# Kernel tuning notes

Measured on AMD Instinct MI355X. Metric: run time of the kernel, lower is better.

The kernel has to match this reference:

```python
import jax, jax.numpy as jnp
import numpy as np

N, F, V, E = 16384, 39, 100000, 16
H1, H2 = 400, 400
EPS = 1e-5

def setup_inputs() -> dict:
    key = jax.random.key(0)
    ks = jax.random.split(key, 12)
    xi = jax.random.randint(ks[0], (N, F, 1), 0, V)  # indices per field
    xv = jax.random.uniform(ks[1], (N, F), dtype=jnp.float32)
    # stacked per-field embedding tables (each table has V+1 rows)
    emb1 = jax.random.normal(ks[2], (F, V + 1), dtype=jnp.float32)          # 1st-order
    emb2 = jax.random.normal(ks[3], (F, V + 1, E), dtype=jnp.float32)       # 2nd-order
    D = F * E
    W1 = jax.random.normal(ks[4], (D, H1), dtype=jnp.float32) / np.sqrt(D)
    b1 = jnp.zeros((H1,), jnp.float32)
    g1 = jnp.ones((H1,), jnp.float32)
    be1 = jnp.zeros((H1,), jnp.float32)
    W2 = jax.random.normal(ks[5], (H1, H2), dtype=jnp.float32) / np.sqrt(H1)
    b2 = jnp.zeros((H2,), jnp.float32)
    g2 = jnp.ones((H2,), jnp.float32)
    be2 = jnp.zeros((H2,), jnp.float32)
    bias = jax.random.normal(ks[6], (1,), dtype=jnp.float32)
    return dict(xi=xi, xv=xv, emb1=emb1, emb2=emb2, W1=W1, b1=b1, g1=g1, be1=be1,
                W2=W2, b2=b2, g2=g2, be2=be2, bias=bias)

def _batchnorm(x, g, b):
    # BatchNorm1d in training mode: batch mean/var (biased)
    mu = x.mean(0)
    var = x.var(0)
    return g * (x - mu) * jax.lax.rsqrt(var + EPS) + b

def reference(xi, xv, emb1, emb2, W1, b1, g1, be1, W2, b2, g2, be2, bias):
    idx = xi[:, :, 0]                     # (N, F)
    f_ids = jnp.arange(F)[None, :]        # (1, F)
    e1 = emb1[f_ids, idx] * xv            # (N, F): per-field 1st-order term
    e2 = emb2[f_ids, idx] * xv[:, :, None]  # (N, F, E)
    s = e2.sum(axis=1)                    # (N, E) sum of embeddings
    fm2 = 0.5 * (s * s - (e2 * e2).sum(axis=1))  # (N, E) FM 2nd-order
    deep = e2.reshape(e2.shape[0], F * E)
    h = _batchnorm(deep @ W1 + b1, g1, be1)       # dropout = identity (eval)
    h = _batchnorm(h @ W2 + b2, g2, be2)
    return e1.sum(axis=1) + fm2.sum(axis=1) + h.sum(axis=1) + bias[0]
```

## Files before the change

### kernel.cpp

```cpp
#include <hip/hip_runtime.h>
#include <hip/hip_bf16.h>

#define Nn 16384
#define Ff 39
#define Vv 100000
#define Ee 16
#define Dd 624
#define KP1 640
#define KP2 448
#define Hh 400
#define EPSf 1e-5f

typedef short short8 __attribute__((ext_vector_type(8)));
typedef float floatx4 __attribute__((ext_vector_type(4)));

__device__ __forceinline__ unsigned short f2bu(float x) {
  __hip_bfloat16 h = __float2bfloat16(x);
  return *reinterpret_cast<unsigned short*>(&h);
}
__device__ __forceinline__ float bf2f(unsigned short v) {
  union { unsigned int u; float f; } x; x.u = ((unsigned int)v) << 16; return x.f;
}

__device__ __forceinline__ void gload16(void* lds, const void* g) {
  __builtin_amdgcn_global_load_lds(
      (const __attribute__((address_space(1))) unsigned int*)g,
      (__attribute__((address_space(3))) unsigned int*)lds, 16, 0, 0);
}

__global__ __launch_bounds__(256) void embed_kernel(
    const int* __restrict__ xi, const float* __restrict__ xv,
    const float* __restrict__ emb1, const float* __restrict__ emb2,
    const float* __restrict__ bias, const float* __restrict__ W1,
    __hip_bfloat16* __restrict__ deep, float* __restrict__ p,
    __hip_bfloat16* __restrict__ W1t, float* __restrict__ stats,
    __hip_bfloat16* __restrict__ x1b) {
  const int b = blockIdx.x;
  __shared__ float Tt[64][65];
  __shared__ int   sidx[4][40];
  __shared__ float sxv[4][40];
  if (b < 70) {
    const int tk = b / 7, tn = b % 7;
    const int k0 = tk * 64, n0 = tn * 64;
    const int c = threadIdx.x & 63, r0 = (threadIdx.x >> 6) * 16;
    const int n = n0 + c;
    #pragma unroll
    for (int r = r0; r < r0 + 16; ++r) {
      const int k = k0 + r;
      Tt[c][r] = (k < Dd && n < Hh) ? W1[(size_t)k * Hh + n] : 0.f;
    }
    __syncthreads();
    const int nl = threadIdx.x >> 2, kq = (threadIdx.x & 3) * 16;
    const int nw = n0 + nl;
    if (nw < Hh) {
      #pragma unroll
      for (int q = 0; q < 4; ++q) {
        const int kk = kq + q * 4;
        *(ushort4*)&W1t[(size_t)nw * KP1 + k0 + kk] = make_ushort4(
            f2bu(Tt[nl][kk]), f2bu(Tt[nl][kk + 1]),
            f2bu(Tt[nl][kk + 2]), f2bu(Tt[nl][kk + 3]));
      }
    }
    return;
  }
  if (b == 70) {
    for (int i = threadIdx.x; i < 2000; i += 256) stats[i] = 0.f;
    return;
  }
  const int w = threadIdx.x >> 6;
  const int lane = threadIdx.x & 63;
  const int n = (b - 71) * 4 + w;
  if (lane < Ff) {
    sidx[w][lane] = xi[n * Ff + lane];
    sxv[w][lane]  = xv[n * Ff + lane];
  }
  __syncthreads();

  float e1v = 0.f;
  if (lane < Ff)
    e1v = emb1[(long)lane * (Vv + 1) + sidx[w][lane]] * sxv[w][lane];

  const float4* e2v = (const float4*)emb2;
  float se0 = 0.f, se1 = 0.f, se2 = 0.f, se3 = 0.f;
  float qe0 = 0.f, qe1 = 0.f, qe2 = 0.f, qe3 = 0.f;
  #pragma unroll
  for (int t = 0; t < 3; ++t) {
    const int j4 = lane + t * 64;
    if (j4 < 156) {
      const int f = j4 >> 2;
      float4 v = e2v[((long)f * (Vv + 1) + sidx[w][f]) * 4 + (j4 & 3)];
      const float xf = sxv[w][f];
      v.x *= xf; v.y *= xf; v.z *= xf; v.w *= xf;
      *(ushort4*)&deep[(size_t)n * KP1 + j4 * 4] =
          make_ushort4(f2bu(v.x), f2bu(v.y), f2bu(v.z), f2bu(v.w));
      se0 += v.x; qe0 += v.x * v.x;
      se1 += v.y; qe1 += v.y * v.y;
      se2 += v.z; qe2 += v.z * v.z;
      se3 += v.w; qe3 += v.w * v.w;
    }
  }
  if (lane < 4)  *(ushort4*)&deep[(size_t)n * KP1 + Dd + lane * 4] = make_ushort4(0, 0, 0, 0);
  if (lane < 12) *(ushort4*)&x1b [(size_t)n * KP2 + Hh + lane * 4] = make_ushort4(0, 0, 0, 0);

  #pragma unroll
  for (int d = 4; d < 64; d <<= 1) {
    se0 += __shfl_xor(se0, d); qe0 += __shfl_xor(qe0, d);
    se1 += __shfl_xor(se1, d); qe1 += __shfl_xor(qe1, d);
    se2 += __shfl_xor(se2, d); qe2 += __shfl_xor(qe2, d);
    se3 += __shfl_xor(se3, d); qe3 += __shfl_xor(qe3, d);
  }
  float val = 0.f;
  if (lane < 4)
    val = 0.5f * ((se0 * se0 - qe0) + (se1 * se1 - qe1) +
                  (se2 * se2 - qe2) + (se3 * se3 - qe3));
  val += e1v;
  #pragma unroll
  for (int d = 1; d < 64; d <<= 1) val += __shfl_xor(val, d);
  if (lane == 0) p[n] = val + bias[0];
}

__global__ __launch_bounds__(256) void gemm_bf16(
    const __hip_bfloat16* __restrict__ A, const __hip_bfloat16* __restrict__ Wt,
    const float* __restrict__ bias, __hip_bfloat16* __restrict__ C,
    float* __restrict__ s, float* __restrict__ ss, const int K, const int ldc) {
  __shared__ __align__(16) short As_s[128 * 64];
  __shared__ __align__(16) short Bs_s[80 * 64];
  __shared__ float redS[4][5][16], redQ[4][5][16];
  const int tid = threadIdx.x;
  const int lin = blockIdx.x + blockIdx.y * 5;
  const int v   = (lin & 7) * 80 + (lin >> 3);
  const int n0  = (v % 5) * 80;
  const int m0  = (v / 5) * 128;
  const int w = tid >> 6, lane = tid & 63;
  const int lm = lane & 15, qd = lane >> 4;

  floatx4 acc[2][5];
  #pragma unroll
  for (int i = 0; i < 2; ++i)
    #pragma unroll
    for (int j = 0; j < 5; ++j)
      acc[i][j] = (floatx4){0.f, 0.f, 0.f, 0.f};

  const int nk = K >> 6;
  for (int ks = 0; ks < nk; ++ks) {
    const int k0 = ks << 6;
    #pragma unroll
    for (int j = 0; j < 4; ++j) {
      const int c = tid + j * 256;
      const int m = c >> 3, kc = c & 7;
      gload16(&As_s[c * 8], &A[(size_t)(m0 + m) * K + k0 + ((kc ^ (m & 7)) << 3)]);
    }
    #pragma unroll
    for (int j = 0; j < 3; ++j) {
      const int c = tid + j * 256;
      if (c < 640) {
        const int nn = c >> 3, kc = c & 7;
        gload16(&Bs_s[c * 8], &Wt[(size_t)(n0 + nn) * K + k0 + ((kc ^ (nn & 7)) << 3)]);
      }
    }
    __syncthreads();
    #pragma unroll
    for (int h = 0; h < 2; ++h) {
      const int sl = (h * 32 + qd * 8) >> 3;
      const int r0 = w * 32 + lm, r1 = r0 + 16;
      const short8 a0 = *(const short8*)&As_s[r0 * 64 + ((sl ^ (r0 & 7)) << 3)];
      const short8 a1 = *(const short8*)&As_s[r1 * 64 + ((sl ^ (r1 & 7)) << 3)];
      #pragma unroll
      for (int nt = 0; nt < 5; ++nt) {
        const int rn = nt * 16 + lm;
        const short8 bfr = *(const short8*)&Bs_s[rn * 64 + ((sl ^ (rn & 7)) << 3)];
        acc[0][nt] = __builtin_amdgcn_mfma_f32_16x16x32_bf16(a0, bfr, acc[0][nt], 0, 0, 0);
        acc[1][nt] = __builtin_amdgcn_mfma_f32_16x16x32_bf16(a1, bfr, acc[1][nt], 0, 0, 0);
      }
    }
    __syncthreads();
  }

  const int rb = m0 + w * 32 + qd * 4;
  #pragma unroll
  for (int nt = 0; nt < 5; ++nt) {
    const int col = n0 + nt * 16 + lm;
    const float bc = bias[col];
    float cs = 0.f, cq = 0.f;
    #pragma unroll
    for (int mt = 0; mt < 2; ++mt) {
      #pragma unroll
      for (int r = 0; r < 4; ++r) {
        const float vv = acc[mt][nt][r] + bc;
        float vf = vv;
        if (C) {
          const __hip_bfloat16 hv = __float2bfloat16(vv);
          C[(size_t)(rb + mt * 16 + r) * ldc + col] = hv;
          vf = __bfloat162float(hv);
        }
        cs += vf; cq += vf * vf;
      }
    }
    cs += __shfl_xor(cs, 16); cq += __shfl_xor(cq, 16);
    cs += __shfl_xor(cs, 32); cq += __shfl_xor(cq, 32);
    if (lane < 16) { redS[w][nt][lm] = cs; redQ[w][nt][lm] = cq; }
  }
  __syncthreads();
  if (tid < 80) {
    const int nt = tid >> 4, l = tid & 15;
    const int col = n0 + nt * 16 + l;
    atomicAdd(&s[col],  redS[0][nt][l] + redS[1][nt][l] + redS[2][nt][l] + redS[3][nt][l]);
    atomicAdd(&ss[col], redQ[0][nt][l] + redQ[1][nt][l] + redQ[2][nt][l] + redQ[3][nt][l]);
  }
}

__global__ __launch_bounds__(256) void prep2_kernel(
    const float* __restrict__ W2,
    const float* __restrict__ s1, const float* __restrict__ ss1,
    const float* __restrict__ g1, const float* __restrict__ be1,
    const float* __restrict__ b2, __hip_bfloat16* __restrict__ W2t, float* __restrict__ b2p) {
  __shared__ float sa[64], sc[64];
  __shared__ float Tt[64][65];
  __shared__ float pcs[256];
  const int tb = blockIdx.x;
  const int tk = tb / 7, tn = tb % 7;
  const int k0 = tk * 64, n0 = tn * 64;
  const int t = threadIdx.x;
  if (t < 64) {
    const int k = k0 + t;
    float a = 0.f, cv = 0.f;
    if (k < Hh) {
      const float mu = s1[k] * (1.f / Nn);
      const float var = ss1[k] * (1.f / Nn) - mu * mu;
      a = g1[k] * rsqrtf(var + EPSf);
      cv = be1[k] - a * mu;
    }
    sa[t] = a; sc[t] = cv;
  }
  __syncthreads();
  const int c = t & 63, r0 = (t >> 6) * 16;
  const int n = n0 + c;
  float pc = 0.f;
  #pragma unroll
  for (int r = r0; r < r0 + 16; ++r) {
    const int k = k0 + r;
    const float wv = (k < Hh && n < Hh) ? W2[(size_t)k * Hh + n] : 0.f;
    Tt[c][r] = sa[r] * wv;
    pc += sc[r] * wv;
  }
  pcs[t] = pc;
  __syncthreads();
  if (t < 64 && n0 + t < Hh) {
    float tot = pcs[t] + pcs[t + 64] + pcs[t + 128] + pcs[t + 192];
    if (k0 == 0) tot += b2[n0 + t];
    atomicAdd(&b2p[n0 + t], tot);
  }
  const int nl = t >> 2, kq = (t & 3) * 16;
  const int nw = n0 + nl;
  if (nw < Hh) {
    #pragma unroll
    for (int q = 0; q < 4; ++q) {
      const int kk = kq + q * 4;
      *(ushort4*)&W2t[(size_t)nw * KP2 + k0 + kk] = make_ushort4(
          f2bu(Tt[nl][kk]), f2bu(Tt[nl][kk + 1]),
          f2bu(Tt[nl][kk + 2]), f2bu(Tt[nl][kk + 3]));
    }
  }
}

__global__ __launch_bounds__(256) void prep3_kernel(
    const __hip_bfloat16* __restrict__ W2t,
    const float* __restrict__ s2, const float* __restrict__ ss2,
    const float* __restrict__ g2, const float* __restrict__ be2,
    const float* __restrict__ b2p, float* __restrict__ u) {
  __shared__ float sal[Hh];
  __shared__ float part[4][64];
  __shared__ float red[256];
  const int t = threadIdx.x;
  float cpart = 0.f;
  for (int h = t; h < Hh; h += 256) {
    const float mu = s2[h] * (1.f / Nn);
    const float var = ss2[h] * (1.f / Nn) - mu * mu;
    const float al = g2[h] * rsqrtf(var + EPSf);
    sal[h] = al;
    cpart += be2[h] - al * mu + al * b2p[h];
  }
  __syncthreads();
  const int k = blockIdx.x * 64 + (t & 63);
  const int hs = t >> 6;
  float acc = 0.f;
  for (int h = hs * 100; h < hs * 100 + 100; ++h)
    acc += sal[h] * bf2f(*(const unsigned short*)&W2t[(size_t)h * KP2 + k]);
  part[hs][t & 63] = acc;
  __syncthreads();
  if (t < 64) u[blockIdx.x * 64 + t] = part[0][t] + part[1][t] + part[2][t] + part[3][t];
  if (blockIdx.x == 0) {
    red[t] = cpart;
    __syncthreads();
    for (int d = 128; d > 0; d >>= 1) { if (t < d) red[t] += red[t + d]; __syncthreads(); }
    if (t == 0) u[KP2] = red[0];
  }
}

__global__ __launch_bounds__(256) void final_kernel(
    const __hip_bfloat16* __restrict__ x1, const float* __restrict__ u,
    const float* __restrict__ p, float* __restrict__ out) {
  __shared__ float su[KP2];
  __shared__ float scc;
  const int t = threadIdx.x;
  for (int i = t; i < KP2; i += 256) su[i] = u[i];
  if (t == 0) scc = u[KP2];
  __syncthreads();
  const int w = t >> 6, lane = t & 63;
  const int n = blockIdx.x * 4 + w;
  const unsigned short* row = (const unsigned short*)(x1 + (size_t)n * KP2);
  float acc = 0.f;
  #pragma unroll
  for (int h0 = lane * 4; h0 < KP2; h0 += 256) {
    const ushort4 uv = *(const ushort4*)&row[h0];
    acc += bf2f(uv.x) * su[h0]     + bf2f(uv.y) * su[h0 + 1]
         + bf2f(uv.z) * su[h0 + 2] + bf2f(uv.w) * su[h0 + 3];
  }
  #pragma unroll
  for (int d = 1; d < 64; d <<= 1) acc += __shfl_xor(acc, d);
  if (lane == 0) out[n] = p[n] + acc + scc;
}

extern "C" void kernel_launch(void* const* d_in, const int* in_sizes, int n_in,
                              void* d_out, int out_size, void* d_ws, size_t ws_size,
                              hipStream_t stream) {
  const int*   xi   = (const int*)d_in[0];
  const float* xv   = (const float*)d_in[1];
  const float* emb1 = (const float*)d_in[2];
  const float* emb2 = (const float*)d_in[3];
  const float* W1   = (const float*)d_in[4];
  const float* b1   = (const float*)d_in[5];
  const float* g1   = (const float*)d_in[6];
  const float* be1  = (const float*)d_in[7];
  const float* W2   = (const float*)d_in[8];
  const float* b2   = (const float*)d_in[9];
  const float* g2   = (const float*)d_in[10];
  const float* be2  = (const float*)d_in[11];
  const float* bias = (const float*)d_in[12];
  float* out = (float*)d_out;

  char* ws = (char*)d_ws;
  __hip_bfloat16* deep = (__hip_bfloat16*)ws;  ws += (size_t)Nn * KP1 * 2;
  __hip_bfloat16* x1b  = (__hip_bfloat16*)ws;  ws += (size_t)Nn * KP2 * 2;
  __hip_bfloat16* W1t  = (__hip_bfloat16*)ws;  ws += (size_t)Hh * KP1 * 2;
  __hip_bfloat16* W2t  = (__hip_bfloat16*)ws;  ws += (size_t)Hh * KP2 * 2;
  float* p    = (float*)ws;  ws += (size_t)Nn * 4;
  float* s1   = (float*)ws;  ws += Hh * 4;
  float* ss1  = (float*)ws;  ws += Hh * 4;
  float* s2   = (float*)ws;  ws += Hh * 4;
  float* ss2  = (float*)ws;  ws += Hh * 4;
  float* b2p  = (float*)ws;  ws += Hh * 4;
  float* u    = (float*)ws;  ws += (KP2 + 1) * 4;

  embed_kernel<<<4167, 256, 0, stream>>>(xi, xv, emb1, emb2, bias, W1, deep, p, W1t, s1, x1b);
  gemm_bf16<<<dim3(5, Nn / 128), 256, 0, stream>>>(deep, W1t, b1, x1b, s1, ss1, KP1, KP2);
  prep2_kernel<<<49, 256, 0, stream>>>(W2, s1, ss1, g1, be1, b2, W2t, b2p);
  gemm_bf16<<<dim3(5, Nn / 128), 256, 0, stream>>>(x1b, W2t, b2p, nullptr, s2, ss2, KP2, 0);
  prep3_kernel<<<7, 256, 0, stream>>>(W2t, s2, ss2, g2, be2, b2p, u);
  final_kernel<<<Nn / 4, 256, 0, stream>>>(x1b, u, p, out);
}
```

Before: 387.7 us.

## Fuse all stages into one persistent kernel with software grid barriers

Replaces the six separate kernel launches with a single persistent kernel of 512 blocks. Atomic-counter grid barriers separate the embedding, first GEMM, BN prep, second GEMM, second prep and final reduction phases. Stats and barrier counters are zeroed with a memset before the launch. The aim is to remove launch gaps and tail effects between stages. In exchange, each phase gets a fixed grid (640 GEMM tiles over 512 blocks leaves an uneven second wave), and the spin barriers need all blocks to be co-resident.

```diff
diff --git a/kernel.cpp b/kernel.cpp
--- a/kernel.cpp
+++ b/kernel.cpp
@@ -10,6 +10,7 @@
 #define KP2 448
 #define Hh 400
 #define EPSf 1e-5f
+#define GRIDB 512
 
 typedef short short8 __attribute__((ext_vector_type(8)));
 typedef float floatx4 __attribute__((ext_vector_type(4)));
@@ -21,116 +22,39 @@
 __device__ __forceinline__ float bf2f(unsigned short v) {
   union { unsigned int u; float f; } x; x.u = ((unsigned int)v) << 16; return x.f;
 }
-
 __device__ __forceinline__ void gload16(void* lds, const void* g) {
   __builtin_amdgcn_global_load_lds(
       (const __attribute__((address_space(1))) unsigned int*)g,
       (__attribute__((address_space(3))) unsigned int*)lds, 16, 0, 0);
 }
 
-__global__ __launch_bounds__(256) void embed_kernel(
-    const int* __restrict__ xi, const float* __restrict__ xv,
-    const float* __restrict__ emb1, const float* __restrict__ emb2,
-    const float* __restrict__ bias, const float* __restrict__ W1,
-    __hip_bfloat16* __restrict__ deep, float* __restrict__ p,
-    __hip_bfloat16* __restrict__ W1t, float* __restrict__ stats,
-    __hip_bfloat16* __restrict__ x1b) {
-  const int b = blockIdx.x;
-  __shared__ float Tt[64][65];
-  __shared__ int   sidx[4][40];
-  __shared__ float sxv[4][40];
-  if (b < 70) {
-    const int tk = b / 7, tn = b % 7;
-    const int k0 = tk * 64, n0 = tn * 64;
-    const int c = threadIdx.x & 63, r0 = (threadIdx.x >> 6) * 16;
-    const int n = n0 + c;
-    #pragma unroll
-    for (int r = r0; r < r0 + 16; ++r) {
-      const int k = k0 + r;
-      Tt[c][r] = (k < Dd && n < Hh) ? W1[(size_t)k * Hh + n] : 0.f;
-    }
-    __syncthreads();
-    const int nl = threadIdx.x >> 2, kq = (threadIdx.x & 3) * 16;
-    const int nw = n0 + nl;
-    if (nw < Hh) {
-      #pragma unroll
-      for (int q = 0; q < 4; ++q) {
-        const int kk = kq + q * 4;
-        *(ushort4*)&W1t[(size_t)nw * KP1 + k0 + kk] = make_ushort4(
-            f2bu(Tt[nl][kk]), f2bu(Tt[nl][kk + 1]),
-            f2bu(Tt[nl][kk + 2]), f2bu(Tt[nl][kk + 3]));
-      }
-    }
-    return;
-  }
-  if (b == 70) {
-    for (int i = threadIdx.x; i < 2000; i += 256) stats[i] = 0.f;
-    return;
-  }
-  const int w = threadIdx.x >> 6;
-  const int lane = threadIdx.x & 63;
-  const int n = (b - 71) * 4 + w;
-  if (lane < Ff) {
-    sidx[w][lane] = xi[n * Ff + lane];
-    sxv[w][lane]  = xv[n * Ff + lane];
-  }
-  __syncthreads();
-
-  float e1v = 0.f;
-  if (lane < Ff)
-    e1v = emb1[(long)lane * (Vv + 1) + sidx[w][lane]] * sxv[w][lane];
-
-  const float4* e2v = (const float4*)emb2;
-  float se0 = 0.f, se1 = 0.f, se2 = 0.f, se3 = 0.f;
-  float qe0 = 0.f, qe1 = 0.f, qe2 = 0.f, qe3 = 0.f;
-  #pragma unroll
-  for (int t = 0; t < 3; ++t) {
-    const int j4 = lane + t * 64;
-    if (j4 < 156) {
-      const int f = j4 >> 2;
-      float4 v = e2v[((long)f * (Vv + 1) + sidx[w][f]) * 4 + (j4 & 3)];
-      const float xf = sxv[w][f];
-      v.x *= xf; v.y *= xf; v.z *= xf; v.w *= xf;
-      *(ushort4*)&deep[(size_t)n * KP1 + j4 * 4] =
-          make_ushort4(f2bu(v.x), f2bu(v.y), f2bu(v.z), f2bu(v.w));
-      se0 += v.x; qe0 += v.x * v.x;
-      se1 += v.y; qe1 += v.y * v.y;
-      se2 += v.z; qe2 += v.z * v.z;
-      se3 += v.w; qe3 += v.w * v.w;
-    }
-  }
-  if (lane < 4)  *(ushort4*)&deep[(size_t)n * KP1 + Dd + lane * 4] = make_ushort4(0, 0, 0, 0);
-  if (lane < 12) *(ushort4*)&x1b [(size_t)n * KP2 + Hh + lane * 4] = make_ushort4(0, 0, 0, 0);
-
-  #pragma unroll
-  for (int d = 4; d < 64; d <<= 1) {
-    se0 += __shfl_xor(se0, d); qe0 += __shfl_xor(qe0, d);
-    se1 += __shfl_xor(se1, d); qe1 += __shfl_xor(qe1, d);
-    se2 += __shfl_xor(se2, d); qe2 += __shfl_xor(qe2, d);
-    se3 += __shfl_xor(se3, d); qe3 += __shfl_xor(qe3, d);
-  }
-  float val = 0.f;
-  if (lane < 4)
-    val = 0.5f * ((se0 * se0 - qe0) + (se1 * se1 - qe1) +
-                  (se2 * se2 - qe2) + (se3 * se3 - qe3));
-  val += e1v;
-  #pragma unroll
-  for (int d = 1; d < 64; d <<= 1) val += __shfl_xor(val, d);
-  if (lane == 0) p[n] = val + bias[0];
-}
-
-__global__ __launch_bounds__(256) void gemm_bf16(
+__device__ __forceinline__ void gridbar(unsigned* bar, int id) {
+  __syncthreads();
+  if (threadIdx.x == 0) {
+    __threadfence();
+    unsigned prev = atomicAdd(&bar[id], 1u);
+    if (prev + 1u < (unsigned)GRIDB) {
+      while (atomicAdd(&bar[id], 0u) < (unsigned)GRIDB)
+        __builtin_amdgcn_s_sleep(2);
+    }
+    __threadfence();
+  }
+  __syncthreads();
+}
+
+__device__ __forceinline__ void gemm_body(
     const __hip_bfloat16* __restrict__ A, const __hip_bfloat16* __restrict__ Wt,
     const float* __restrict__ bias, __hip_bfloat16* __restrict__ C,
-    float* __restrict__ s, float* __restrict__ ss, const int K, const int ldc) {
-  __shared__ __align__(16) short As_s[128 * 64];
-  __shared__ __align__(16) short Bs_s[80 * 64];
-  __shared__ float redS[4][5][16], redQ[4][5][16];
+    float* __restrict__ s, float* __restrict__ ss, const int K, const int ldc,
+    char* smem, const int tile) {
+  short* As_s = (short*)smem;
+  short* Bs_s = (short*)(smem + 16384);
+  float* redS = (float*)(smem + 16384 + 10240);
+  float* redQ = redS + 320;
   const int tid = threadIdx.x;
-  const int lin = blockIdx.x + blockIdx.y * 5;
-  const int v   = (lin & 7) * 80 + (lin >> 3);
-  const int n0  = (v % 5) * 80;
-  const int m0  = (v / 5) * 128;
+  const int v  = (tile & 7) * 80 + (tile >> 3);
+  const int n0 = (v % 5) * 80;
+  const int m0 = (v / 5) * 128;
   const int w = tid >> 6, lane = tid & 63;
   const int lm = lane & 15, qd = lane >> 4;
 
@@ -161,7 +85,7 @@
     __syncthreads();
     #pragma unroll
     for (int h = 0; h < 2; ++h) {
-      const int sl = (h * 32 + qd * 8) >> 3;
+      const int sl = h * 4 + qd;
       const int r0 = w * 32 + lm, r1 = r0 + 16;
       const short8 a0 = *(const short8*)&As_s[r0 * 64 + ((sl ^ (r0 & 7)) << 3)];
       const short8 a1 = *(const short8*)&As_s[r1 * 64 + ((sl ^ (r1 & 7)) << 3)];
@@ -198,26 +122,26 @@
     }
     cs += __shfl_xor(cs, 16); cq += __shfl_xor(cq, 16);
     cs += __shfl_xor(cs, 32); cq += __shfl_xor(cq, 32);
-    if (lane < 16) { redS[w][nt][lm] = cs; redQ[w][nt][lm] = cq; }
+    if (lane < 16) { redS[w * 80 + nt * 16 + lm] = cs; redQ[w * 80 + nt * 16 + lm] = cq; }
   }
   __syncthreads();
   if (tid < 80) {
     const int nt = tid >> 4, l = tid & 15;
     const int col = n0 + nt * 16 + l;
-    atomicAdd(&s[col],  redS[0][nt][l] + redS[1][nt][l] + redS[2][nt][l] + redS[3][nt][l]);
-    atomicAdd(&ss[col], redQ[0][nt][l] + redQ[1][nt][l] + redQ[2][nt][l] + redQ[3][nt][l]);
-  }
-}
-
-__global__ __launch_bounds__(256) void prep2_kernel(
-    const float* __restrict__ W2,
-    const float* __restrict__ s1, const float* __restrict__ ss1,
-    const float* __restrict__ g1, const float* __restrict__ be1,
-    const float* __restrict__ b2, __hip_bfloat16* __restrict__ W2t, float* __restrict__ b2p) {
-  __shared__ float sa[64], sc[64];
-  __shared__ float Tt[64][65];
-  __shared__ float pcs[256];
-  const int tb = blockIdx.x;
+    const int o = nt * 16 + l;
+    atomicAdd(&s[col],  redS[o] + redS[80 + o] + redS[160 + o] + redS[240 + o]);
+    atomicAdd(&ss[col], redQ[o] + redQ[80 + o] + redQ[160 + o] + redQ[240 + o]);
+  }
+}
+
+__device__ __forceinline__ void prep2_body(
+    const float* __restrict__ W2, const float* __restrict__ s1, const float* __restrict__ ss1,
+    const float* __restrict__ g1, const float* __restrict__ be1, const float* __restrict__ b2,
+    __hip_bfloat16* __restrict__ W2t, float* __restrict__ b2p, char* smem, const int tb) {
+  float* sa = (float*)smem;
+  float* sc = sa + 64;
+  float (*Tt)[65] = (float(*)[65])(smem + 512);
+  float* pcs = (float*)(smem + 512 + 16640);
   const int tk = tb / 7, tn = tb % 7;
   const int k0 = tk * 64, n0 = tn * 64;
   const int t = threadIdx.x;
@@ -263,14 +187,14 @@
   }
 }
 
-__global__ __launch_bounds__(256) void prep3_kernel(
-    const __hip_bfloat16* __restrict__ W2t,
-    const float* __restrict__ s2, const float* __restrict__ ss2,
-    const float* __restrict__ g2, const float* __restrict__ be2,
-    const float* __restrict__ b2p, float* __restrict__ u) {
-  __shared__ float sal[Hh];
-  __shared__ float part[4][64];
-  __shared__ float red[256];
+__device__ __forceinline__ void prep3_body(
+    const __hip_bfloat16* __restrict__ W2t, const float* __restrict__ s2,
+    const float* __restrict__ ss2, const float* __restrict__ g2,
+    const float* __restrict__ be2, const float* __restrict__ b2p,
+    float* __restrict__ u, char* smem, const int blk) {
+  float* sal  = (float*)smem;
+  float* part = sal + Hh;
+  float* red  = part + 256;
   const int t = threadIdx.x;
   float cpart = 0.f;
   for (int h = t; h < Hh; h += 256) {
@@ -281,15 +205,15 @@
     cpart += be2[h] - al * mu + al * b2p[h];
   }
   __syncthreads();
-  const int k = blockIdx.x * 64 + (t & 63);
+  const int k = blk * 64 + (t & 63);
   const int hs = t >> 6;
   float acc = 0.f;
   for (int h = hs * 100; h < hs * 100 + 100; ++h)
     acc += sal[h] * bf2f(*(const unsigned short*)&W2t[(size_t)h * KP2 + k]);
-  part[hs][t & 63] = acc;
-  __syncthreads();
-  if (t < 64) u[blockIdx.x * 64 + t] = part[0][t] + part[1][t] + part[2][t] + part[3][t];
-  if (blockIdx.x == 0) {
+  part[hs * 64 + (t & 63)] = acc;
+  __syncthreads();
+  if (t < 64) u[blk * 64 + t] = part[t] + part[64 + t] + part[128 + t] + part[192 + t];
+  if (blk == 0) {
     red[t] = cpart;
     __syncthreads();
     for (int d = 128; d > 0; d >>= 1) { if (t < d) red[t] += red[t + d]; __syncthreads(); }
@@ -297,28 +221,143 @@
   }
 }
 
-__global__ __launch_bounds__(256) void final_kernel(
-    const __hip_bfloat16* __restrict__ x1, const float* __restrict__ u,
-    const float* __restrict__ p, float* __restrict__ out) {
-  __shared__ float su[KP2];
-  __shared__ float scc;
-  const int t = threadIdx.x;
-  for (int i = t; i < KP2; i += 256) su[i] = u[i];
-  if (t == 0) scc = u[KP2];
-  __syncthreads();
-  const int w = t >> 6, lane = t & 63;
-  const int n = blockIdx.x * 4 + w;
-  const unsigned short* row = (const unsigned short*)(x1 + (size_t)n * KP2);
-  float acc = 0.f;
-  #pragma unroll
-  for (int h0 = lane * 4; h0 < KP2; h0 += 256) {
-    const ushort4 uv = *(const ushort4*)&row[h0];
-    acc += bf2f(uv.x) * su[h0]     + bf2f(uv.y) * su[h0 + 1]
-         + bf2f(uv.z) * su[h0 + 2] + bf2f(uv.w) * su[h0 + 3];
-  }
-  #pragma unroll
-  for (int d = 1; d < 64; d <<= 1) acc += __shfl_xor(acc, d);
-  if (lane == 0) out[n] = p[n] + acc + scc;
+__global__ __launch_bounds__(256, 2) void fused(
+    const int* __restrict__ xi, const float* __restrict__ xv,
+    const float* __restrict__ emb1, const float* __restrict__ emb2,
+    const float* __restrict__ W1, const float* __restrict__ b1,
+    const float* __restrict__ g1, const float* __restrict__ be1,
+    const float* __restrict__ W2, const float* __restrict__ b2,
+    const float* __restrict__ g2, const float* __restrict__ be2,
+    const float* __restrict__ bias, float* __restrict__ out,
+    __hip_bfloat16* __restrict__ deep, __hip_bfloat16* __restrict__ x1b,
+    __hip_bfloat16* __restrict__ W1t, __hip_bfloat16* __restrict__ W2t,
+    float* __restrict__ p, float* __restrict__ stats, float* __restrict__ u,
+    unsigned* __restrict__ bar) {
+  __shared__ __align__(16) char smem[29184];
+  const int blk = blockIdx.x, tid = threadIdx.x;
+  const int w = tid >> 6, lane = tid & 63;
+  float* s1  = stats;
+  float* ss1 = stats + 400;
+  float* s2  = stats + 800;
+  float* ss2 = stats + 1200;
+  float* b2p = stats + 1600;
+
+  if (blk < 70) {
+    float (*Tt)[65] = (float(*)[65])smem;
+    const int tk = blk / 7, tn = blk % 7;
+    const int k0 = tk * 64, n0 = tn * 64;
+    const int c = tid & 63, r0 = (tid >> 6) * 16;
+    const int n = n0 + c;
+    #pragma unroll
+    for (int r = r0; r < r0 + 16; ++r) {
+      const int k = k0 + r;
+      Tt[c][r] = (k < Dd && n < Hh) ? W1[(size_t)k * Hh + n] : 0.f;
+    }
+    __syncthreads();
+    const int nl = tid >> 2, kq = (tid & 3) * 16;
+    const int nw = n0 + nl;
+    if (nw < Hh) {
+      #pragma unroll
+      for (int q = 0; q < 4; ++q) {
+        const int kk = kq + q * 4;
+        *(ushort4*)&W1t[(size_t)nw * KP1 + k0 + kk] = make_ushort4(
+            f2bu(Tt[nl][kk]), f2bu(Tt[nl][kk + 1]),
+            f2bu(Tt[nl][kk + 2]), f2bu(Tt[nl][kk + 3]));
+      }
+    }
+  }
+  {
+    int*   sidx = (int*)smem;
+    float* sxv  = (float*)(smem + 640);
+    const float4* e2v = (const float4*)emb2;
+    const float bias0 = bias[0];
+    for (int g = blk; g < 4096; g += GRIDB) {
+      __syncthreads();
+      const int n = g * 4 + w;
+      if (lane < Ff) {
+        sidx[w * 40 + lane] = xi[n * Ff + lane];
+        sxv [w * 40 + lane] = xv[n * Ff + lane];
+      }
+      __syncthreads();
+      float e1v = 0.f;
+      if (lane < Ff)
+        e1v = emb1[(long)lane * (Vv + 1) + sidx[w * 40 + lane]] * sxv[w * 40 + lane];
+
+      float se0 = 0.f, se1 = 0.f, se2 = 0.f, se3 = 0.f;
+      float qe0 = 0.f, qe1 = 0.f, qe2 = 0.f, qe3 = 0.f;
+      #pragma unroll
+      for (int t = 0; t < 3; ++t) {
+        const int j4 = lane + t * 64;
+        if (j4 < 156) {
+          const int f = j4 >> 2;
+          float4 v = e2v[((long)f * (Vv + 1) + sidx[w * 40 + f]) * 4 + (j4 & 3)];
+          const float xf = sxv[w * 40 + f];
+          v.x *= xf; v.y *= xf; v.z *= xf; v.w *= xf;
+          *(ushort4*)&deep[(size_t)n * KP1 + j4 * 4] =
+              make_ushort4(f2bu(v.x), f2bu(v.y), f2bu(v.z), f2bu(v.w));
+          se0 += v.x; qe0 += v.x * v.x;
+          se1 += v.y; qe1 += v.y * v.y;
+          se2 += v.z; qe2 += v.z * v.z;
+          se3 += v.w; qe3 += v.w * v.w;
+        }
+      }
+      if (lane < 4)  *(ushort4*)&deep[(size_t)n * KP1 + Dd + lane * 4] = make_ushort4(0, 0, 0, 0);
+      if (lane < 12) *(ushort4*)&x1b [(size_t)n * KP2 + Hh + lane * 4] = make_ushort4(0, 0, 0, 0);
+
+      #pragma unroll
+      for (int d = 4; d < 64; d <<= 1) {
+        se0 += __shfl_xor(se0, d); qe0 += __shfl_xor(qe0, d);
+        se1 += __shfl_xor(se1, d); qe1 += __shfl_xor(qe1, d);
+        se2 += __shfl_xor(se2, d); qe2 += __shfl_xor(qe2, d);
+        se3 += __shfl_xor(se3, d); qe3 += __shfl_xor(qe3, d);
+      }
+      float val = 0.f;
+      if (lane < 4)
+        val = 0.5f * ((se0 * se0 - qe0) + (se1 * se1 - qe1) +
+                      (se2 * se2 - qe2) + (se3 * se3 - qe3));
+      val += e1v;
+      #pragma unroll
+      for (int d = 1; d < 64; d <<= 1) val += __shfl_xor(val, d);
+      if (lane == 0) p[n] = val + bias0;
+    }
+  }
+  gridbar(bar, 0);
+
+  for (int t = blk; t < 640; t += GRIDB)
+    gemm_body(deep, W1t, b1, x1b, s1, ss1, KP1, KP2, smem, t);
+  gridbar(bar, 1);
+
+  if (blk < 49) prep2_body(W2, s1, ss1, g1, be1, b2, W2t, b2p, smem, blk);
+  gridbar(bar, 2);
+
+  for (int t = blk; t < 640; t += GRIDB)
+    gemm_body(x1b, W2t, b2p, nullptr, s2, ss2, KP2, 0, smem, t);
+  gridbar(bar, 3);
+
+  if (blk < 7) prep3_body(W2t, s2, ss2, g2, be2, b2p, u, smem, blk);
+  gridbar(bar, 4);
+
+  {
+    float* su = (float*)smem;
+    __syncthreads();
+    for (int i = tid; i < KP2 + 1; i += 256) su[i] = u[i];
+    __syncthreads();
+    const float cc = su[KP2];
+    for (int g = blk; g < 4096; g += GRIDB) {
+      const int n = g * 4 + w;
+      const unsigned short* row = (const unsigned short*)(x1b + (size_t)n * KP2);
+      float acc = 0.f;
+      #pragma unroll
+      for (int h0 = lane * 4; h0 < KP2; h0 += 256) {
+        const ushort4 uv = *(const ushort4*)&row[h0];
+        acc += bf2f(uv.x) * su[h0]     + bf2f(uv.y) * su[h0 + 1]
+             + bf2f(uv.z) * su[h0 + 2] + bf2f(uv.w) * su[h0 + 3];
+      }
+      #pragma unroll
+      for (int d = 1; d < 64; d <<= 1) acc += __shfl_xor(acc, d);
+      if (lane == 0) out[n] = p[n] + acc + cc;
+    }
+  }
 }
 
 extern "C" void kernel_launch(void* const* d_in, const int* in_sizes, int n_in,
@@ -344,18 +383,13 @@
   __hip_bfloat16* x1b  = (__hip_bfloat16*)ws;  ws += (size_t)Nn * KP2 * 2;
   __hip_bfloat16* W1t  = (__hip_bfloat16*)ws;  ws += (size_t)Hh * KP1 * 2;
   __hip_bfloat16* W2t  = (__hip_bfloat16*)ws;  ws += (size_t)Hh * KP2 * 2;
-  float* p    = (float*)ws;  ws += (size_t)Nn * 4;
-  float* s1   = (float*)ws;  ws += Hh * 4;
-  float* ss1  = (float*)ws;  ws += Hh * 4;
-  float* s2   = (float*)ws;  ws += Hh * 4;
-  float* ss2  = (float*)ws;  ws += Hh * 4;
-  float* b2p  = (float*)ws;  ws += Hh * 4;
-  float* u    = (float*)ws;  ws += (KP2 + 1) * 4;
-
-  embed_kernel<<<4167, 256, 0, stream>>>(xi, xv, emb1, emb2, bias, W1, deep, p, W1t, s1, x1b);
-  gemm_bf16<<<dim3(5, Nn / 128), 256, 0, stream>>>(deep, W1t, b1, x1b, s1, ss1, KP1, KP2);
-  prep2_kernel<<<49, 256, 0, stream>>>(W2, s1, ss1, g1, be1, b2, W2t, b2p);
-  gemm_bf16<<<dim3(5, Nn / 128), 256, 0, stream>>>(x1b, W2t, b2p, nullptr, s2, ss2, KP2, 0);
-  prep3_kernel<<<7, 256, 0, stream>>>(W2t, s2, ss2, g2, be2, b2p, u);
-  final_kernel<<<Nn / 4, 256, 0, stream>>>(x1b, u, p, out);
-}
+  float* p     = (float*)ws;  ws += (size_t)Nn * 4;
+  float* stats = (float*)ws;  ws += 2000 * 4;
+  float* u     = (float*)ws;  ws += 449 * 4;
+  unsigned* bar = (unsigned*)ws; ws += 8 * 4;
+
+  hipMemsetAsync(stats, 0, (2000 + 449 + 8) * 4, stream);
+  fused<<<GRIDB, 256, 0, stream>>>(xi, xv, emb1, emb2, W1, b1, g1, be1,
+                                   W2, b2, g2, be2, bias, out,
+                                   deep, x1b, W1t, W2t, p, stats, u, bar);
+}
```

Result: slower. 587.4 us (+51.5%).

## Fold BN-prep kernels into GEMM launches as tail blocks gated by completion counter

Applied to the files above, without the earlier changes.

Removes the separate prep2 and prep3 launches by appending extra blocks to each GEMM grid. Those blocks spin on an atomic done counter until all 640 tile blocks have published their column statistics, then run the prep work. The goal is to save two kernel launches and their inter-kernel gaps. The risk is spin-waiting blocks occupying CUs, and deadlock if the tail blocks were ever scheduled before the work blocks. Shared memory is unified into one char buffer and the stats layout is contiguous so a single zeroing pass also clears the counters.

```diff
diff --git a/kernel.cpp b/kernel.cpp
--- a/kernel.cpp
+++ b/kernel.cpp
@@ -10,6 +10,7 @@
 #define KP2 448
 #define Hh 400
 #define EPSf 1e-5f
+#define NWORK 640
 
 typedef short short8 __attribute__((ext_vector_type(8)));
 typedef float floatx4 __attribute__((ext_vector_type(4)));
@@ -21,7 +22,6 @@
 __device__ __forceinline__ float bf2f(unsigned short v) {
   union { unsigned int u; float f; } x; x.u = ((unsigned int)v) << 16; return x.f;
 }
-
 __device__ __forceinline__ void gload16(void* lds, const void* g) {
   __builtin_amdgcn_global_load_lds(
       (const __attribute__((address_space(1))) unsigned int*)g,
@@ -64,7 +64,7 @@
     return;
   }
   if (b == 70) {
-    for (int i = threadIdx.x; i < 2000; i += 256) stats[i] = 0.f;
+    for (int i = threadIdx.x; i < 2008; i += 256) stats[i] = 0.f;
     return;
   }
   const int w = threadIdx.x >> 6;
@@ -119,15 +119,124 @@
   if (lane == 0) p[n] = val + bias[0];
 }
 
+__device__ __forceinline__ void prep2_body(
+    const float* __restrict__ W2, const float* __restrict__ s1, const float* __restrict__ ss1,
+    const float* __restrict__ g1, const float* __restrict__ be1, const float* __restrict__ b2,
+    __hip_bfloat16* __restrict__ W2t, float* __restrict__ b2p, char* smem, const int tb) {
+  float* sa = (float*)smem;
+  float* sc = sa + 64;
+  float (*Tt)[65] = (float(*)[65])(smem + 512);
+  float* pcs = (float*)(smem + 512 + 16640);
+  const int tk = tb / 7, tn = tb % 7;
+  const int k0 = tk * 64, n0 = tn * 64;
+  const int t = threadIdx.x;
+  if (t < 64) {
+    const int k = k0 + t;
+    float a = 0.f, cv = 0.f;
+    if (k < Hh) {
+      const float mu = s1[k] * (1.f / Nn);
+      const float var = ss1[k] * (1.f / Nn) - mu * mu;
+      a = g1[k] * rsqrtf(var + EPSf);
+      cv = be1[k] - a * mu;
+    }
+    sa[t] = a; sc[t] = cv;
+  }
+  __syncthreads();
+  const int c = t & 63, r0 = (t >> 6) * 16;
+  const int n = n0 + c;
+  float pc = 0.f;
+  #pragma unroll
+  for (int r = r0; r < r0 + 16; ++r) {
+    const int k = k0 + r;
+    const float wv = (k < Hh && n < Hh) ? W2[(size_t)k * Hh + n] : 0.f;
+    Tt[c][r] = sa[r] * wv;
+    pc += sc[r] * wv;
+  }
+  pcs[t] = pc;
+  __syncthreads();
+  if (t < 64 && n0 + t < Hh) {
+    float tot = pcs[t] + pcs[t + 64] + pcs[t + 128] + pcs[t + 192];
+    if (k0 == 0) tot += b2[n0 + t];
+    atomicAdd(&b2p[n0 + t], tot);
+  }
+  const int nl = t >> 2, kq = (t & 3) * 16;
+  const int nw = n0 + nl;
+  if (nw < Hh) {
+    #pragma unroll
+    for (int q = 0; q < 4; ++q) {
+      const int kk = kq + q * 4;
+      *(ushort4*)&W2t[(size_t)nw * KP2 + k0 + kk] = make_ushort4(
+          f2bu(Tt[nl][kk]), f2bu(Tt[nl][kk + 1]),
+          f2bu(Tt[nl][kk + 2]), f2bu(Tt[nl][kk + 3]));
+    }
+  }
+}
+
+__device__ __forceinline__ void prep3_body(
+    const __hip_bfloat16* __restrict__ W2t, const float* __restrict__ s2,
+    const float* __restrict__ ss2, const float* __restrict__ g2,
+    const float* __restrict__ be2, const float* __restrict__ b2p,
+    float* __restrict__ u, char* smem, const int blk) {
+  float* sal  = (float*)smem;
+  float* part = sal + Hh;
+  float* red  = part + 256;
+  const int t = threadIdx.x;
+  float cpart = 0.f;
+  for (int h = t; h < Hh; h += 256) {
+    const float mu = s2[h] * (1.f / Nn);
+    const float var = ss2[h] * (1.f / Nn) - mu * mu;
+    const float al = g2[h] * rsqrtf(var + EPSf);
+    sal[h] = al;
+    cpart += be2[h] - al * mu + al * b2p[h];
+  }
+  __syncthreads();
+  const int k = blk * 64 + (t & 63);
+  const int hs = t >> 6;
+  float acc = 0.f;
+  for (int h = hs * 100; h < hs * 100 + 100; ++h)
+    acc += sal[h] * bf2f(*(const unsigned short*)&W2t[(size_t)h * KP2 + k]);
+  part[hs * 64 + (t & 63)] = acc;
+  __syncthreads();
+  if (t < 64) u[blk * 64 + t] = part[t] + part[64 + t] + part[128 + t] + part[192 + t];
+  if (blk == 0) {
+    red[t] = cpart;
+    __syncthreads();
+    for (int d = 128; d > 0; d >>= 1) { if (t < d) red[t] += red[t + d]; __syncthreads(); }
+    if (t == 0) u[KP2] = red[0];
+  }
+}
+
 __global__ __launch_bounds__(256) void gemm_bf16(
     const __hip_bfloat16* __restrict__ A, const __hip_bfloat16* __restrict__ Wt,
     const float* __restrict__ bias, __hip_bfloat16* __restrict__ C,
-    float* __restrict__ s, float* __restrict__ ss, const int K, const int ldc) {
-  __shared__ __align__(16) short As_s[128 * 64];
-  __shared__ __align__(16) short Bs_s[80 * 64];
-  __shared__ float redS[4][5][16], redQ[4][5][16];
+    float* __restrict__ s, float* __restrict__ ss, const int K, const int ldc,
+    const int tailMode, unsigned* __restrict__ done,
+    const float* __restrict__ W2, const float* __restrict__ gA,
+    const float* __restrict__ beA, const float* __restrict__ b2,
+    __hip_bfloat16* __restrict__ W2t, float* __restrict__ b2p,
+    float* __restrict__ u) {
+  __shared__ __align__(16) char smem[29184];
   const int tid = threadIdx.x;
-  const int lin = blockIdx.x + blockIdx.y * 5;
+
+  if (blockIdx.x >= NWORK) {
+    if (tid == 0) {
+      while (atomicAdd(done, 0u) < (unsigned)NWORK) __builtin_amdgcn_s_sleep(16);
+      __threadfence();
+    }
+    __syncthreads();
+    const int tt = blockIdx.x - NWORK;
+    if (tailMode == 1)
+      prep2_body(W2, s, ss, gA, beA, b2, W2t, b2p, smem, tt);
+    else
+      prep3_body(W2t, s, ss, gA, beA, b2p, u, smem, tt);
+    return;
+  }
+
+  short* As_s = (short*)smem;
+  short* Bs_s = (short*)(smem + 16384);
+  float* redS = (float*)(smem + 16384 + 10240);
+  float* redQ = redS + 320;
+  const int lin = blockIdx.x;
   const int v   = (lin & 7) * 80 + (lin >> 3);
   const int n0  = (v % 5) * 80;
   const int m0  = (v / 5) * 128;
@@ -161,7 +270,7 @@
     __syncthreads();
     #pragma unroll
     for (int h = 0; h < 2; ++h) {
-      const int sl = (h * 32 + qd * 8) >> 3;
+      const int sl = h * 4 + qd;
       const int r0 = w * 32 + lm, r1 = r0 + 16;
       const short8 a0 = *(const short8*)&As_s[r0 * 64 + ((sl ^ (r0 & 7)) << 3)];
       const short8 a1 = *(const short8*)&As_s[r1 * 64 + ((sl ^ (r1 & 7)) << 3)];
@@ -198,102 +307,21 @@
     }
     cs += __shfl_xor(cs, 16); cq += __shfl_xor(cq, 16);
     cs += __shfl_xor(cs, 32); cq += __shfl_xor(cq, 32);
-    if (lane < 16) { redS[w][nt][lm] = cs; redQ[w][nt][lm] = cq; }
+    if (lane < 16) { redS[w * 80 + nt * 16 + lm] = cs; redQ[w * 80 + nt * 16 + lm] = cq; }
   }
   __syncthreads();
   if (tid < 80) {
     const int nt = tid >> 4, l = tid & 15;
     const int col = n0 + nt * 16 + l;
-    atomicAdd(&s[col],  redS[0][nt][l] + redS[1][nt][l] + redS[2][nt][l] + redS[3][nt][l]);
-    atomicAdd(&ss[col], redQ[0][nt][l] + redQ[1][nt][l] + redQ[2][nt][l] + redQ[3][nt][l]);
-  }
-}
-
-__global__ __launch_bounds__(256) void prep2_kernel(
-    const float* __restrict__ W2,
-    const float* __restrict__ s1, const float* __restrict__ ss1,
-    const float* __restrict__ g1, const float* __restrict__ be1,
-    const float* __restrict__ b2, __hip_bfloat16* __restrict__ W2t, float* __restrict__ b2p) {
-  __shared__ float sa[64], sc[64];
-  __shared__ float Tt[64][65];
-  __shared__ float pcs[256];
-  const int tb = blockIdx.x;
-  const int tk = tb / 7, tn = tb % 7;
-  const int k0 = tk * 64, n0 = tn * 64;
-  const int t = threadIdx.x;
-  if (t < 64) {
-    const int k = k0 + t;
-    float a = 0.f, cv = 0.f;
-    if (k < Hh) {
-      const float mu = s1[k] * (1.f / Nn);
-      const float var = ss1[k] * (1.f / Nn) - mu * mu;
-      a = g1[k] * rsqrtf(var + EPSf);
-      cv = be1[k] - a * mu;
-    }
-    sa[t] = a; sc[t] = cv;
-  }
-  __syncthreads();
-  const int c = t & 63, r0 = (t >> 6) * 16;
-  const int n = n0 + c;
-  float pc = 0.f;
-  #pragma unroll
-  for (int r = r0; r < r0 + 16; ++r) {
-    const int k = k0 + r;
-    const float wv = (k < Hh && n < Hh) ? W2[(size_t)k * Hh + n] : 0.f;
-    Tt[c][r] = sa[r] * wv;
-    pc += sc[r] * wv;
-  }
-  pcs[t] = pc;
-  __syncthreads();
-  if (t < 64 && n0 + t < Hh) {
-    float tot = pcs[t] + pcs[t + 64] + pcs[t + 128] + pcs[t + 192];
-    if (k0 == 0) tot += b2[n0 + t];
-    atomicAdd(&b2p[n0 + t], tot);
-  }
-  const int nl = t >> 2, kq = (t & 3) * 16;
-  const int nw = n0 + nl;
-  if (nw < Hh) {
-    #pragma unroll
-    for (int q = 0; q < 4; ++q) {
-      const int kk = kq + q * 4;
-      *(ushort4*)&W2t[(size_t)nw * KP2 + k0 + kk] = make_ushort4(
-          f2bu(Tt[nl][kk]), f2bu(Tt[nl][kk + 1]),
-          f2bu(Tt[nl][kk + 2]), f2bu(Tt[nl][kk + 3]));
-    }
-  }
-}
-
-__global__ __launch_bounds__(256) void prep3_kernel(
-    const __hip_bfloat16* __restrict__ W2t,
-    const float* __restrict__ s2, const float* __restrict__ ss2,
-    const float* __restrict__ g2, const float* __restrict__ be2,
-    const float* __restrict__ b2p, float* __restrict__ u) {
-  __shared__ float sal[Hh];
-  __shared__ float part[4][64];
-  __shared__ float red[256];
-  const int t = threadIdx.x;
-  float cpart = 0.f;
-  for (int h = t; h < Hh; h += 256) {
-    const float mu = s2[h] * (1.f / Nn);
-    const float var = ss2[h] * (1.f / Nn) - mu * mu;
-    const float al = g2[h] * rsqrtf(var + EPSf);
-    sal[h] = al;
-    cpart += be2[h] - al * mu + al * b2p[h];
-  }
-  __syncthreads();
-  const int k = blockIdx.x * 64 + (t & 63);
-  const int hs = t >> 6;
-  float acc = 0.f;
-  for (int h = hs * 100; h < hs * 100 + 100; ++h)
-    acc += sal[h] * bf2f(*(const unsigned short*)&W2t[(size_t)h * KP2 + k]);
-  part[hs][t & 63] = acc;
-  __syncthreads();
-  if (t < 64) u[blockIdx.x * 64 + t] = part[0][t] + part[1][t] + part[2][t] + part[3][t];
-  if (blockIdx.x == 0) {
-    red[t] = cpart;
-    __syncthreads();
-    for (int d = 128; d > 0; d >>= 1) { if (t < d) red[t] += red[t + d]; __syncthreads(); }
-    if (t == 0) u[KP2] = red[0];
+    const int o = nt * 16 + l;
+    float o1 = atomicAdd(&s[col],  redS[o] + redS[80 + o] + redS[160 + o] + redS[240 + o]);
+    float o2 = atomicAdd(&ss[col], redQ[o] + redQ[80 + o] + redQ[160 + o] + redQ[240 + o]);
+    __asm__ volatile("" :: "v"(o1), "v"(o2));
+  }
+  __syncthreads();
+  if (tid == 0) {
+    __threadfence();
+    atomicAdd(done, 1u);
   }
 }
 
@@ -344,18 +372,21 @@
   __hip_bfloat16* x1b  = (__hip_bfloat16*)ws;  ws += (size_t)Nn * KP2 * 2;
   __hip_bfloat16* W1t  = (__hip_bfloat16*)ws;  ws += (size_t)Hh * KP1 * 2;
   __hip_bfloat16* W2t  = (__hip_bfloat16*)ws;  ws += (size_t)Hh * KP2 * 2;
-  float* p    = (float*)ws;  ws += (size_t)Nn * 4;
-  float* s1   = (float*)ws;  ws += Hh * 4;
-  float* ss1  = (float*)ws;  ws += Hh * 4;
-  float* s2   = (float*)ws;  ws += Hh * 4;
-  float* ss2  = (float*)ws;  ws += Hh * 4;
-  float* b2p  = (float*)ws;  ws += Hh * 4;
-  float* u    = (float*)ws;  ws += (KP2 + 1) * 4;
-
-  embed_kernel<<<4167, 256, 0, stream>>>(xi, xv, emb1, emb2, bias, W1, deep, p, W1t, s1, x1b);
-  gemm_bf16<<<dim3(5, Nn / 128), 256, 0, stream>>>(deep, W1t, b1, x1b, s1, ss1, KP1, KP2);
-  prep2_kernel<<<49, 256, 0, stream>>>(W2, s1, ss1, g1, be1, b2, W2t, b2p);
-  gemm_bf16<<<dim3(5, Nn / 128), 256, 0, stream>>>(x1b, W2t, b2p, nullptr, s2, ss2, KP2, 0);
-  prep3_kernel<<<7, 256, 0, stream>>>(W2t, s2, ss2, g2, be2, b2p, u);
+  float* p     = (float*)ws;  ws += (size_t)Nn * 4;
+  float* stats = (float*)ws;  ws += 2008 * 4;
+  float* u     = (float*)ws;  ws += 449 * 4;
+
+  float* s1  = stats;
+  float* ss1 = stats + 400;
+  float* s2  = stats + 800;
+  float* ss2 = stats + 1200;
+  float* b2p = stats + 1600;
+  unsigned* done = (unsigned*)(stats + 2000);
+
+  embed_kernel<<<4167, 256, 0, stream>>>(xi, xv, emb1, emb2, bias, W1, deep, p, W1t, stats, x1b);
+  gemm_bf16<<<NWORK + 49, 256, 0, stream>>>(deep, W1t, b1, x1b, s1, ss1, KP1, KP2,
+                                            1, done + 0, W2, g1, be1, b2, W2t, b2p, u);
+  gemm_bf16<<<NWORK + 7, 256, 0, stream>>>(x1b, W2t, b2p, nullptr, s2, ss2, KP2, 0,
+                                           2, done + 1, W2, g2, be2, b2, W2t, b2p, u);
   final_kernel<<<Nn / 4, 256, 0, stream>>>(x1b, u, p, out);
 }
```

Measured after the change: 418.8 us. 1.08x slower.
